# Kernel tuning notes

Hardware: AMD Instinct MI355X
Metric: run time of the kernel (lower is better)

## Reference

```python
import jax, jax.numpy as jnp
import numpy as np

NUM_HEADS = 16
EMBED_DIM = 1024
HEAD_DIM = EMBED_DIM // NUM_HEADS
SCALE = HEAD_DIM * -0.5  # faithful to source: multiplicative, negative


def setup_inputs() -> dict:
    key = jax.random.key(0)
    kx, kq, kk, kv, ko = jax.random.split(key, 5)
    B, S, E = 2, 2048, EMBED_DIM
    std = 1.0 / np.sqrt(E)
    return {
        "x": jax.random.normal(kx, (B, S, E), dtype=jnp.float32),
        "Wq": jax.random.normal(kq, (E, E), dtype=jnp.float32) * std,
        "Wk": jax.random.normal(kk, (E, E), dtype=jnp.float32) * std,
        "Wv": jax.random.normal(kv, (E, E), dtype=jnp.float32) * std,
        "Wo": jax.random.normal(ko, (E, E), dtype=jnp.float32) * std,
    }


def reference(x, Wq, Wk, Wv, Wo):
    B, S, E = x.shape
    H, D = NUM_HEADS, HEAD_DIM
    # nn.Linear(bias=False): y = x @ W.T
    q = (x @ Wq.T).reshape(B, S, H, D).transpose(0, 2, 1, 3)  # unused downstream (faithful to source)
    k = (x @ Wk.T).reshape(B, S, H, D).transpose(0, 2, 1, 3)  # [B,H,S,D]
    v = (x @ Wv.T).reshape(B, S, H, D).transpose(0, 2, 1, 3)
    # Source bug reproduced: logits = K @ V^T, scaled by head_dim * -0.5
    logits = jnp.einsum('bhsd,bhtd->bhst', k, v) * SCALE  # [B,H,S,S]
    attn = jax.nn.softmax(logits, axis=-1)
    out = jnp.einsum('bhst,bhtd->bhsd', attn, v)  # [B,H,S,D]
    out = out.transpose(0, 2, 1, 3).reshape(B, S, E)
    return out @ Wo.T
```

## Files before the change

### kernel.cpp

```cpp
#include <hip/hip_runtime.h>
#include <math.h>

#define B_ 2
#define S_ 2048
#define E_ 1024
#define H_ 16
#define D_ 64
#define M_ (B_ * S_)
#define SC2 (-46.166241308446828f)

typedef unsigned short u16;
typedef _Float16 f16;
typedef __attribute__((ext_vector_type(8))) _Float16 f16x8;
typedef __attribute__((ext_vector_type(2))) __fp16 fp16x2_n;
typedef __attribute__((ext_vector_type(16))) float f32x16;

static __device__ __forceinline__ f32x16 mfma_h(f16x8 a, f16x8 b, f32x16 c) {
    return __builtin_amdgcn_mfma_f32_32x32x16_f16(a, b, c, 0, 0, 0);
}
static __device__ __forceinline__ u16 f16bits(f16 h) {
    union { f16 h; u16 u; } c; c.h = h; return c.u;
}
static __device__ __forceinline__ unsigned pack2(u16 a, u16 b) {
    return (unsigned)a | ((unsigned)b << 16);
}
static __device__ __forceinline__ unsigned pkrtz(float a, float b) {
    fp16x2_n h = __builtin_amdgcn_cvt_pkrtz(a, b);
    unsigned u; __builtin_memcpy(&u, &h, 4); return u;
}
#define ROWMAP(r, hh) (((r) & 3) + ((((r) >> 2)) << 3) + ((hh) << 2))

__global__ __launch_bounds__(256)
void convert_split(const float* __restrict__ x, const float* __restrict__ Wk,
                   const float* __restrict__ Wv, const float* __restrict__ Wo,
                   u16* __restrict__ Xh, u16* __restrict__ Xl,
                   u16* __restrict__ Wkh, u16* __restrict__ Wkl,
                   u16* __restrict__ Wvh, u16* __restrict__ Wvl,
                   u16* __restrict__ Woh, u16* __restrict__ Wol)
{
    const int blk = blockIdx.x;
    const float* src; u16 *dh, *dl; int base; float sc = 1.0f;
    if (blk < 4096)      { src = x;  dh = Xh;  dl = Xl;  base = blk; }
    else if (blk < 5120) { src = Wk; dh = Wkh; dl = Wkl; base = blk - 4096; sc = SC2; }
    else if (blk < 6144) { src = Wv; dh = Wvh; dl = Wvl; base = blk - 5120; }
    else                 { src = Wo; dh = Woh; dl = Wol; base = blk - 6144; }
    const size_t off = ((size_t)base * 256 + threadIdx.x) * 4;
    const float4 v = *(const float4*)(src + off);
    const float f[4] = {v.x * sc, v.y * sc, v.z * sc, v.w * sc};
    u16 h4[4], l4[4];
#pragma unroll
    for (int i = 0; i < 4; ++i) {
        const f16 h = (f16)f[i];
        h4[i] = f16bits(h);
        l4[i] = f16bits((f16)(f[i] - (float)h));
    }
    *(uint2*)(dh + off) = make_uint2(pack2(h4[0], h4[1]), pack2(h4[2], h4[3]));
    *(uint2*)(dl + off) = make_uint2(pack2(l4[0], l4[1]), pack2(l4[2], l4[3]));
}

#define CSB 1032
#define ARR (4 * CSB)

template<int MODE>
__global__ __launch_bounds__(256, 1)
void gemm_f(const u16* __restrict__ Ah_, const u16* __restrict__ Al_,
            const u16* __restrict__ B1h_, const u16* __restrict__ B1l_,
            const u16* __restrict__ B2h_, const u16* __restrict__ B2l_,
            u16* __restrict__ Khg, u16* __restrict__ Klg,
            u16* __restrict__ Vhg, u16* __restrict__ Vtg,
            float* __restrict__ Cout)
{
    constexpr int NARR = (MODE == 0 ? 6 : 2);
    __shared__ u16 stage[NARR * ARR];

    const int tid = threadIdx.x;
    const int w = tid >> 6, l31 = tid & 31, hh = (tid >> 5) & 1;
    const int ws = w >> 1;
    const int wn = (w & 1) << 6;
    const int m0 = blockIdx.y * 128, n0 = blockIdx.x * 128;
    const int ch8 = (ws << 1) + hh;

    const int sr = tid >> 1, c0 = (tid & 1) << 1;
    const size_t gA = (size_t)(m0 + sr) * E_ + (c0 << 3);
    const size_t gB = (size_t)(n0 + sr) * E_ + (c0 << 3);
    const int lo0 = c0 * CSB + sr * 8;
    const int lo1 = (c0 + 1) * CSB + sr * 8;

    f32x16 acc1[4][2], acc2[4][2];
#pragma unroll
    for (int mt = 0; mt < 4; ++mt)
#pragma unroll
        for (int nt = 0; nt < 2; ++nt)
#pragma unroll
            for (int r = 0; r < 16; ++r) {
                acc1[mt][nt][r] = 0.f;
                if constexpr (MODE == 0) acc2[mt][nt][r] = 0.f;
            }

    f16x8 pf[2 * NARR];
    const u16* gptr[6];
    gptr[0] = Ah_; gptr[1] = Al_; gptr[2] = B1h_;
    gptr[3] = B1l_; gptr[4] = B2h_; gptr[5] = B2l_;

    auto load_tile = [&](int k0) {
#pragma unroll
        for (int a = 0; a < NARR; ++a) {
            const size_t g = ((MODE == 0 && a < 2) || (MODE == 1 && a < 1)) ? gA : gB;
            const u16* p = (MODE == 1 && a == 1) ? B1h_ : gptr[a];
            pf[2 * a + 0] = *(const f16x8*)(p + g + k0);
            pf[2 * a + 1] = *(const f16x8*)(p + g + k0 + 8);
        }
    };
    auto store_tile = [&]() {
#pragma unroll
        for (int a = 0; a < NARR; ++a) {
            *(f16x8*)&stage[a * ARR + lo0] = pf[2 * a + 0];
            *(f16x8*)&stage[a * ARR + lo1] = pf[2 * a + 1];
        }
    };

    load_tile(0);
    for (int it = 0; it < 32; ++it) {
        store_tile();
        __syncthreads();
        if (it + 1 < 32) load_tile((it + 1) << 5);

        f16x8 xh[4], xl[4];
#pragma unroll
        for (int mt = 0; mt < 4; ++mt) {
            const int off = ch8 * CSB + ((mt << 5) + l31) * 8;
            xh[mt] = *(const f16x8*)&stage[0 * ARR + off];
            if constexpr (MODE == 0)
                xl[mt] = *(const f16x8*)&stage[1 * ARR + off];
        }
#pragma unroll
        for (int nt = 0; nt < 2; ++nt) {
            const int boff = ch8 * CSB + (wn + (nt << 5) + l31) * 8;
            if constexpr (MODE == 0) {
                const f16x8 b1h = *(const f16x8*)&stage[2 * ARR + boff];
                const f16x8 b1l = *(const f16x8*)&stage[3 * ARR + boff];
                const f16x8 b2h = *(const f16x8*)&stage[4 * ARR + boff];
                const f16x8 b2l = *(const f16x8*)&stage[5 * ARR + boff];
#pragma unroll
                for (int mt = 0; mt < 4; ++mt) {
                    acc1[mt][nt] = mfma_h(xh[mt], b1h, acc1[mt][nt]);
                    acc1[mt][nt] = mfma_h(xh[mt], b1l, acc1[mt][nt]);
                    acc1[mt][nt] = mfma_h(xl[mt], b1h, acc1[mt][nt]);
                    acc2[mt][nt] = mfma_h(xh[mt], b2h, acc2[mt][nt]);
                    acc2[mt][nt] = mfma_h(xh[mt], b2l, acc2[mt][nt]);
                    acc2[mt][nt] = mfma_h(xl[mt], b2h, acc2[mt][nt]);
                }
            } else {
                const f16x8 b1h = *(const f16x8*)&stage[1 * ARR + boff];
#pragma unroll
                for (int mt = 0; mt < 4; ++mt)
                    acc1[mt][nt] = mfma_h(xh[mt], b1h, acc1[mt][nt]);
            }
        }
        __syncthreads();
    }

    float* red = (float*)stage;
#pragma unroll
    for (int ai = 0; ai < (MODE == 0 ? 2 : 1); ++ai) {
#pragma unroll
        for (int mt = 0; mt < 4; ++mt) {
            __syncthreads();
            if (ws == 1) {
#pragma unroll
                for (int nt = 0; nt < 2; ++nt)
#pragma unroll
                    for (int r = 0; r < 16; ++r)
                        red[ROWMAP(r, hh) * 128 + wn + (nt << 5) + l31] =
                            (ai == 0) ? acc1[mt][nt][r] : acc2[mt][nt][r];
            }
            __syncthreads();
            if (ws == 0) {
#pragma unroll
                for (int nt = 0; nt < 2; ++nt)
#pragma unroll
                    for (int r = 0; r < 16; ++r) {
                        const float p = red[ROWMAP(r, hh) * 128 + wn + (nt << 5) + l31];
                        if (ai == 0) acc1[mt][nt][r] += p; else acc2[mt][nt][r] += p;
                    }
            }
        }
    }
    if (ws != 0) return;

#pragma unroll
    for (int nt = 0; nt < 2; ++nt) {
        const int n = n0 + wn + (nt << 5) + l31;
        if constexpr (MODE == 1) {
#pragma unroll
            for (int mt = 0; mt < 4; ++mt)
#pragma unroll
                for (int r = 0; r < 16; ++r) {
                    const int m = m0 + (mt << 5) + ROWMAP(r, hh);
                    Cout[(size_t)m * E_ + n] = acc1[mt][nt][r];
                }
        } else {
            const int hd = n >> 6, d = n & 63;
            const int b = m0 >> 11;
#pragma unroll
            for (int mt = 0; mt < 4; ++mt) {
                u16 vb[16];
#pragma unroll
                for (int r = 0; r < 16; ++r) {
                    const int s = (m0 + (mt << 5) + ROWMAP(r, hh)) & (S_ - 1);
                    const size_t ib = (((size_t)(b * H_ + hd) << 11) + s) * D_ + d;
                    const float kv = acc1[mt][nt][r];
                    const f16 kh = (f16)kv;
                    Khg[ib] = f16bits(kh);
                    Klg[ib] = f16bits((f16)(kv - (float)kh));
                    const f16 vh = (f16)acc2[mt][nt][r];
                    vb[r] = f16bits(vh);
                    Vhg[ib] = vb[r];
                }
                const size_t vtb = ((size_t)(b * H_ + hd) * D_ + d) << 11;
#pragma unroll
                for (int g = 0; g < 4; ++g) {
                    const int s0 = ((m0 + (mt << 5)) & (S_ - 1)) + (g << 3) + (hh << 2);
                    *(uint2*)&Vtg[vtb + s0] =
                        make_uint2(pack2(vb[4 * g], vb[4 * g + 1]),
                                   pack2(vb[4 * g + 2], vb[4 * g + 3]));
                }
            }
        }
    }
}

#define CSA 520
#define VA  (8 * CSA)
#define CSP 264
#define PW  (8 * CSP)

__global__ __launch_bounds__(512, 2)
void attn_mfma(const u16* __restrict__ Kh, const u16* __restrict__ Kl,
               const u16* __restrict__ Vh, const u16* __restrict__ Vt,
               u16* __restrict__ Obuf)
{
    __shared__ u16 sV[2 * VA];
    __shared__ u16 sP[8][PW];
    __shared__ float Alpha[8][32], Linv[8][32];

    const int tid = threadIdx.x;
    const int w = tid >> 6, l31 = tid & 31, hh = (tid >> 5) & 1;
    const int bh = blockIdx.y;
    const int sbase = blockIdx.x * 256 + (w << 5);
    const int sg = sbase + l31;

    f16x8 kfh[4], kfl[4];
    {
        const size_t kb = ((size_t)bh * S_ + sg) * D_;
#pragma unroll
        for (int ks = 0; ks < 4; ++ks) {
            const int db = (ks << 4) + (hh << 3);
            kfh[ks] = *(const f16x8*)(Kh + kb + db);
            kfl[ks] = *(const f16x8*)(Kl + kb + db);
        }
    }

    f32x16 oacc[2];
#pragma unroll
    for (int r = 0; r < 16; ++r) { oacc[0][r] = 0.f; oacc[1][r] = 0.f; }
    float m_i = -INFINITY, l_i = 0.f;

    const int rr = tid >> 3, cc = tid & 7;
    const size_t gn = ((size_t)bh * S_ + rr) * D_ + (cc << 3);
    const size_t gt = ((size_t)bh * D_ + rr) * S_ + (cc << 3);
    const int slo = cc * CSA + rr * 8;
    u16* P = &sP[w][0];

    f16x8 pv[2];
    auto load_tile = [&](int t0) {
        pv[0] = *(const f16x8*)(Vh + gn + (size_t)t0 * D_);
        pv[1] = *(const f16x8*)(Vt + gt + t0);
    };

    load_tile(0);
    for (int it = 0; it < 32; ++it) {
        *(f16x8*)&sV[slo] = pv[0];
        *(f16x8*)&sV[VA + slo] = pv[1];
        __syncthreads();
        if (it + 1 < 32) load_tile((it + 1) << 6);

        f32x16 st[2];
#pragma unroll
        for (int r = 0; r < 16; ++r) { st[0][r] = 0.f; st[1][r] = 0.f; }
#pragma unroll
        for (int ks = 0; ks < 4; ++ks) {
            const int ch = (ks << 1) + hh;
#pragma unroll
            for (int mt = 0; mt < 2; ++mt) {
                const f16x8 av = *(const f16x8*)&sV[ch * CSA + ((mt << 5) + l31) * 8];
                st[mt] = mfma_h(av, kfh[ks], st[mt]);
                st[mt] = mfma_h(av, kfl[ks], st[mt]);
            }
        }

        float tmax = -INFINITY;
#pragma unroll
        for (int mt = 0; mt < 2; ++mt)
#pragma unroll
            for (int r = 0; r < 16; ++r) tmax = fmaxf(tmax, st[mt][r]);
        tmax = fmaxf(tmax, __shfl_xor(tmax, 32));
        const float mnew = fmaxf(m_i, tmax);
        const float alpha = __builtin_amdgcn_exp2f(m_i - mnew);
        m_i = mnew;
        const unsigned long long cmask = __ballot(tmax >= mnew - 30.f);

        if (cmask) {
            float rsum = 0.f;
#pragma unroll
            for (int mt = 0; mt < 2; ++mt)
#pragma unroll
                for (int r = 0; r < 16; ++r) {
                    const float p = __builtin_amdgcn_exp2f(st[mt][r] - mnew);
                    st[mt][r] = p;
                    rsum += p;
                }
            rsum += __shfl_xor(rsum, 32);
            l_i = l_i * alpha + rsum;
        }
        if (__ballot(alpha != 1.0f)) {
            if (hh == 0) Alpha[w][l31] = alpha;
#pragma unroll
            for (int g = 0; g < 4; ++g) {
                const float4 av = *(const float4*)&Alpha[w][(g << 3) + (hh << 2)];
                const float af[4] = {av.x, av.y, av.z, av.w};
#pragma unroll
                for (int q = 0; q < 4; ++q) {
                    oacc[0][(g << 2) + q] *= af[q];
                    oacc[1][(g << 2) + q] *= af[q];
                }
            }
        }
        if (cmask) {
#pragma unroll
            for (int mt = 0; mt < 2; ++mt)
#pragma unroll
                for (int g = 0; g < 4; ++g)
                    *(uint2*)&P[((mt << 2) + g) * CSP + l31 * 8 + (hh << 2)] =
                        make_uint2(pkrtz(st[mt][4 * g], st[mt][4 * g + 1]),
                                   pkrtz(st[mt][4 * g + 2], st[mt][4 * g + 3]));
#pragma unroll
            for (int ks = 0; ks < 4; ++ks) {
                const int ch = (ks << 1) + hh;
                const f16x8 pfr = *(const f16x8*)&P[ch * CSP + l31 * 8];
#pragma unroll
                for (int nt = 0; nt < 2; ++nt) {
                    const f16x8 vtf = *(const f16x8*)&sV[VA + ch * CSA + ((nt << 5) + l31) * 8];
                    oacc[nt] = mfma_h(pfr, vtf, oacc[nt]);
                }
            }
        }
        __syncthreads();
    }

    if (hh == 0) Linv[w][l31] = 1.0f / l_i;
    const int b = bh >> 4;
    const int hd = bh & 15;
    u16* Or = Obuf + ((size_t)b * S_ + sbase) * E_ + (hd << 6);
#pragma unroll
    for (int g = 0; g < 4; ++g) {
        const float4 iv = *(const float4*)&Linv[w][(g << 3) + (hh << 2)];
        const float invs[4] = {iv.x, iv.y, iv.z, iv.w};
#pragma unroll
        for (int nt = 0; nt < 2; ++nt)
#pragma unroll
            for (int q = 0; q < 4; ++q) {
                const int sl = (g << 3) + (hh << 2) + q;
                Or[(size_t)sl * E_ + (nt << 5) + l31] =
                    f16bits((f16)(oacc[nt][(g << 2) + q] * invs[q]));
            }
    }
}

extern "C" void kernel_launch(void* const* d_in, const int* in_sizes, int n_in,
                              void* d_out, int out_size, void* d_ws, size_t ws_size,
                              hipStream_t stream)
{
    (void)in_sizes; (void)n_in; (void)out_size; (void)ws_size;
    const float* x  = (const float*)d_in[0];
    const float* Wk = (const float*)d_in[2];
    const float* Wv = (const float*)d_in[3];
    const float* Wo = (const float*)d_in[4];
    float* out = (float*)d_out;

    char* ws = (char*)d_ws;
    const size_t MB = 1u << 20;
    u16* Xh  = (u16*)(ws + 0 * MB);
    u16* Xl  = (u16*)(ws + 8 * MB);
    u16* Wkh = (u16*)(ws + 16 * MB);
    u16* Wkl = (u16*)(ws + 18 * MB);
    u16* Wvh = (u16*)(ws + 20 * MB);
    u16* Wvl = (u16*)(ws + 22 * MB);
    u16* Woh = (u16*)(ws + 24 * MB);
    u16* Kh  = (u16*)(ws + 26 * MB);
    u16* Kl  = (u16*)(ws + 35 * MB);
    u16* Vh  = (u16*)(ws + 44 * MB);
    u16* Vt  = (u16*)(ws + 53 * MB);
    u16* Obuf = Xl;
    u16* Wol_junk = Kh;

    convert_split<<<7168, 256, 0, stream>>>(x, Wk, Wv, Wo,
                                            Xh, Xl, Wkh, Wkl, Wvh, Wvl, Woh, Wol_junk);
    gemm_f<0><<<dim3(E_ / 128, M_ / 128), 256, 0, stream>>>(
        Xh, Xl, Wkh, Wkl, Wvh, Wvl, Kh, Kl, Vh, Vt, nullptr);
    attn_mfma<<<dim3(S_ / 256, B_ * H_), 512, 0, stream>>>(Kh, Kl, Vh, Vt, Obuf);
    gemm_f<1><<<dim3(E_ / 128, M_ / 128), 256, 0, stream>>>(
        Obuf, Obuf, Woh, Woh, Woh, Woh,
        nullptr, nullptr, nullptr, nullptr, out);
}
```

Before: 239.2 us.

## Widen GEMM blocks to 512 threads, split K-score MFMA chains, skip Wo low-part writes

The projection GEMMs now launch 512 threads per block: four warps tile the 128x128 output 2x2 and two K-split groups each own half of every 32-wide K chunk, with a simplified cross-group reduction through shared memory. This gives each warp fewer accumulators and more warps per CU to hide latency, at the cost of an extra reduction pass. In attention, the hi and lo K MFMAs go into separate accumulators that are summed afterwards, which breaks the dependent MFMA chain. The convert kernel also stops writing the unused low half of Wo.

```diff
diff --git a/kernel.cpp b/kernel.cpp
--- a/kernel.cpp
+++ b/kernel.cpp
@@ -36,14 +36,14 @@
                    u16* __restrict__ Xh, u16* __restrict__ Xl,
                    u16* __restrict__ Wkh, u16* __restrict__ Wkl,
                    u16* __restrict__ Wvh, u16* __restrict__ Wvl,
-                   u16* __restrict__ Woh, u16* __restrict__ Wol)
+                   u16* __restrict__ Woh)
 {
     const int blk = blockIdx.x;
-    const float* src; u16 *dh, *dl; int base; float sc = 1.0f;
+    const float* src; u16 *dh, *dl; int base; float sc = 1.0f; bool wantlo = true;
     if (blk < 4096)      { src = x;  dh = Xh;  dl = Xl;  base = blk; }
     else if (blk < 5120) { src = Wk; dh = Wkh; dl = Wkl; base = blk - 4096; sc = SC2; }
     else if (blk < 6144) { src = Wv; dh = Wvh; dl = Wvl; base = blk - 5120; }
-    else                 { src = Wo; dh = Woh; dl = Wol; base = blk - 6144; }
+    else                 { src = Wo; dh = Woh; dl = Woh; base = blk - 6144; wantlo = false; }
     const size_t off = ((size_t)base * 256 + threadIdx.x) * 4;
     const float4 v = *(const float4*)(src + off);
     const float f[4] = {v.x * sc, v.y * sc, v.z * sc, v.w * sc};
@@ -55,40 +55,41 @@
         l4[i] = f16bits((f16)(f[i] - (float)h));
     }
     *(uint2*)(dh + off) = make_uint2(pack2(h4[0], h4[1]), pack2(h4[2], h4[3]));
-    *(uint2*)(dl + off) = make_uint2(pack2(l4[0], l4[1]), pack2(l4[2], l4[3]));
+    if (wantlo)
+        *(uint2*)(dl + off) = make_uint2(pack2(l4[0], l4[1]), pack2(l4[2], l4[3]));
 }
 
 #define CSB 1032
 #define ARR (4 * CSB)
 
 template<int MODE>
-__global__ __launch_bounds__(256, 1)
+__global__ __launch_bounds__(512, 2)
 void gemm_f(const u16* __restrict__ Ah_, const u16* __restrict__ Al_,
-            const u16* __restrict__ B1h_, const u16* __restrict__ B1l_,
-            const u16* __restrict__ B2h_, const u16* __restrict__ B2l_,
+            const u16* __restrict__ Bkh_, const u16* __restrict__ Bkl_,
+            const u16* __restrict__ Bvh_, const u16* __restrict__ Bvl_,
             u16* __restrict__ Khg, u16* __restrict__ Klg,
             u16* __restrict__ Vhg, u16* __restrict__ Vtg,
             float* __restrict__ Cout)
 {
     constexpr int NARR = (MODE == 0 ? 6 : 2);
-    __shared__ u16 stage[NARR * ARR];
+    constexpr int SSZ = (NARR * ARR > 16384 ? NARR * ARR : 16384);
+    __shared__ u16 stage[SSZ];
 
     const int tid = threadIdx.x;
     const int w = tid >> 6, l31 = tid & 31, hh = (tid >> 5) & 1;
-    const int ws = w >> 1;
-    const int wn = (w & 1) << 6;
+    const int wt = w & 3, ws = w >> 2;
+    const int wm = (wt >> 1) << 6, wn = (wt & 1) << 6;
     const int m0 = blockIdx.y * 128, n0 = blockIdx.x * 128;
     const int ch8 = (ws << 1) + hh;
 
-    const int sr = tid >> 1, c0 = (tid & 1) << 1;
-    const size_t gA = (size_t)(m0 + sr) * E_ + (c0 << 3);
-    const size_t gB = (size_t)(n0 + sr) * E_ + (c0 << 3);
-    const int lo0 = c0 * CSB + sr * 8;
-    const int lo1 = (c0 + 1) * CSB + sr * 8;
-
-    f32x16 acc1[4][2], acc2[4][2];
-#pragma unroll
-    for (int mt = 0; mt < 4; ++mt)
+    const int sr = tid >> 2, sch = tid & 3;
+    const size_t gA = (size_t)(m0 + sr) * E_ + (sch << 3);
+    const size_t gB = (size_t)(n0 + sr) * E_ + (sch << 3);
+    const int slo = sch * CSB + sr * 8;
+
+    f32x16 acc1[2][2], acc2[2][2];
+#pragma unroll
+    for (int mt = 0; mt < 2; ++mt)
 #pragma unroll
         for (int nt = 0; nt < 2; ++nt)
 #pragma unroll
@@ -97,26 +98,23 @@
                 if constexpr (MODE == 0) acc2[mt][nt][r] = 0.f;
             }
 
-    f16x8 pf[2 * NARR];
-    const u16* gptr[6];
-    gptr[0] = Ah_; gptr[1] = Al_; gptr[2] = B1h_;
-    gptr[3] = B1l_; gptr[4] = B2h_; gptr[5] = B2l_;
-
+    f16x8 pf[NARR];
     auto load_tile = [&](int k0) {
-#pragma unroll
-        for (int a = 0; a < NARR; ++a) {
-            const size_t g = ((MODE == 0 && a < 2) || (MODE == 1 && a < 1)) ? gA : gB;
-            const u16* p = (MODE == 1 && a == 1) ? B1h_ : gptr[a];
-            pf[2 * a + 0] = *(const f16x8*)(p + g + k0);
-            pf[2 * a + 1] = *(const f16x8*)(p + g + k0 + 8);
+        pf[0] = *(const f16x8*)(Ah_ + gA + k0);
+        if constexpr (MODE == 0) {
+            pf[1] = *(const f16x8*)(Al_ + gA + k0);
+            pf[2] = *(const f16x8*)(Bkh_ + gB + k0);
+            pf[3] = *(const f16x8*)(Bkl_ + gB + k0);
+            pf[4] = *(const f16x8*)(Bvh_ + gB + k0);
+            pf[5] = *(const f16x8*)(Bvl_ + gB + k0);
+        } else {
+            pf[1] = *(const f16x8*)(Bkh_ + gB + k0);
         }
     };
     auto store_tile = [&]() {
 #pragma unroll
-        for (int a = 0; a < NARR; ++a) {
-            *(f16x8*)&stage[a * ARR + lo0] = pf[2 * a + 0];
-            *(f16x8*)&stage[a * ARR + lo1] = pf[2 * a + 1];
-        }
+        for (int a = 0; a < NARR; ++a)
+            *(f16x8*)&stage[a * ARR + slo] = pf[a];
     };
 
     load_tile(0);
@@ -125,65 +123,63 @@
         __syncthreads();
         if (it + 1 < 32) load_tile((it + 1) << 5);
 
-        f16x8 xh[4], xl[4];
-#pragma unroll
-        for (int mt = 0; mt < 4; ++mt) {
-            const int off = ch8 * CSB + ((mt << 5) + l31) * 8;
+        const int co = ch8 * CSB;
+        f16x8 xh[2], xl[2];
+#pragma unroll
+        for (int mt = 0; mt < 2; ++mt) {
+            const int off = co + (wm + (mt << 5) + l31) * 8;
             xh[mt] = *(const f16x8*)&stage[0 * ARR + off];
             if constexpr (MODE == 0)
                 xl[mt] = *(const f16x8*)&stage[1 * ARR + off];
         }
 #pragma unroll
         for (int nt = 0; nt < 2; ++nt) {
-            const int boff = ch8 * CSB + (wn + (nt << 5) + l31) * 8;
+            const int ro = co + (wn + (nt << 5) + l31) * 8;
             if constexpr (MODE == 0) {
-                const f16x8 b1h = *(const f16x8*)&stage[2 * ARR + boff];
-                const f16x8 b1l = *(const f16x8*)&stage[3 * ARR + boff];
-                const f16x8 b2h = *(const f16x8*)&stage[4 * ARR + boff];
-                const f16x8 b2l = *(const f16x8*)&stage[5 * ARR + boff];
-#pragma unroll
-                for (int mt = 0; mt < 4; ++mt) {
-                    acc1[mt][nt] = mfma_h(xh[mt], b1h, acc1[mt][nt]);
-                    acc1[mt][nt] = mfma_h(xh[mt], b1l, acc1[mt][nt]);
-                    acc1[mt][nt] = mfma_h(xl[mt], b1h, acc1[mt][nt]);
-                    acc2[mt][nt] = mfma_h(xh[mt], b2h, acc2[mt][nt]);
-                    acc2[mt][nt] = mfma_h(xh[mt], b2l, acc2[mt][nt]);
-                    acc2[mt][nt] = mfma_h(xl[mt], b2h, acc2[mt][nt]);
+                const f16x8 bkh = *(const f16x8*)&stage[2 * ARR + ro];
+                const f16x8 bkl = *(const f16x8*)&stage[3 * ARR + ro];
+                const f16x8 bvh = *(const f16x8*)&stage[4 * ARR + ro];
+                const f16x8 bvl = *(const f16x8*)&stage[5 * ARR + ro];
+#pragma unroll
+                for (int mt = 0; mt < 2; ++mt) {
+                    acc1[mt][nt] = mfma_h(xh[mt], bkh, acc1[mt][nt]);
+                    acc1[mt][nt] = mfma_h(xh[mt], bkl, acc1[mt][nt]);
+                    acc1[mt][nt] = mfma_h(xl[mt], bkh, acc1[mt][nt]);
+                    acc2[mt][nt] = mfma_h(xh[mt], bvh, acc2[mt][nt]);
+                    acc2[mt][nt] = mfma_h(xh[mt], bvl, acc2[mt][nt]);
+                    acc2[mt][nt] = mfma_h(xl[mt], bvh, acc2[mt][nt]);
                 }
             } else {
-                const f16x8 b1h = *(const f16x8*)&stage[1 * ARR + boff];
-#pragma unroll
-                for (int mt = 0; mt < 4; ++mt)
-                    acc1[mt][nt] = mfma_h(xh[mt], b1h, acc1[mt][nt]);
+                const f16x8 bh = *(const f16x8*)&stage[1 * ARR + ro];
+#pragma unroll
+                for (int mt = 0; mt < 2; ++mt)
+                    acc1[mt][nt] = mfma_h(xh[mt], bh, acc1[mt][nt]);
             }
         }
         __syncthreads();
     }
 
     float* red = (float*)stage;
-#pragma unroll
-    for (int ai = 0; ai < (MODE == 0 ? 2 : 1); ++ai) {
-#pragma unroll
-        for (int mt = 0; mt < 4; ++mt) {
-            __syncthreads();
-            if (ws == 1) {
-#pragma unroll
-                for (int nt = 0; nt < 2; ++nt)
-#pragma unroll
-                    for (int r = 0; r < 16; ++r)
-                        red[ROWMAP(r, hh) * 128 + wn + (nt << 5) + l31] =
-                            (ai == 0) ? acc1[mt][nt][r] : acc2[mt][nt][r];
-            }
-            __syncthreads();
-            if (ws == 0) {
-#pragma unroll
-                for (int nt = 0; nt < 2; ++nt)
-#pragma unroll
-                    for (int r = 0; r < 16; ++r) {
-                        const float p = red[ROWMAP(r, hh) * 128 + wn + (nt << 5) + l31];
-                        if (ai == 0) acc1[mt][nt][r] += p; else acc2[mt][nt][r] += p;
-                    }
-            }
+    constexpr int NR = (MODE == 0 ? 4 : 2);
+#pragma unroll
+    for (int rd = 0; rd < NR; ++rd) {
+        const int mt = rd & 1;
+        f32x16 (*A)[2] = (MODE == 0 && rd >= 2) ? acc2 : acc1;
+        __syncthreads();
+        if (ws == 1) {
+#pragma unroll
+            for (int nt = 0; nt < 2; ++nt)
+#pragma unroll
+                for (int r = 0; r < 16; ++r)
+                    red[(((wt << 1) + nt) << 10) + (r << 6) + (hh << 5) + l31] = A[mt][nt][r];
+        }
+        __syncthreads();
+        if (ws == 0) {
+#pragma unroll
+            for (int nt = 0; nt < 2; ++nt)
+#pragma unroll
+                for (int r = 0; r < 16; ++r)
+                    A[mt][nt][r] += red[(((wt << 1) + nt) << 10) + (r << 6) + (hh << 5) + l31];
         }
     }
     if (ws != 0) return;
@@ -193,37 +189,37 @@
         const int n = n0 + wn + (nt << 5) + l31;
         if constexpr (MODE == 1) {
 #pragma unroll
-            for (int mt = 0; mt < 4; ++mt)
+            for (int mt = 0; mt < 2; ++mt)
 #pragma unroll
                 for (int r = 0; r < 16; ++r) {
-                    const int m = m0 + (mt << 5) + ROWMAP(r, hh);
+                    const int m = m0 + wm + (mt << 5) + ROWMAP(r, hh);
                     Cout[(size_t)m * E_ + n] = acc1[mt][nt][r];
                 }
         } else {
             const int hd = n >> 6, d = n & 63;
             const int b = m0 >> 11;
 #pragma unroll
-            for (int mt = 0; mt < 4; ++mt) {
-                u16 vb[16];
+            for (int mt = 0; mt < 2; ++mt) {
+                u16 vb16[16];
 #pragma unroll
                 for (int r = 0; r < 16; ++r) {
-                    const int s = (m0 + (mt << 5) + ROWMAP(r, hh)) & (S_ - 1);
+                    const int s = (m0 + wm + (mt << 5) + ROWMAP(r, hh)) & (S_ - 1);
                     const size_t ib = (((size_t)(b * H_ + hd) << 11) + s) * D_ + d;
                     const float kv = acc1[mt][nt][r];
                     const f16 kh = (f16)kv;
                     Khg[ib] = f16bits(kh);
                     Klg[ib] = f16bits((f16)(kv - (float)kh));
                     const f16 vh = (f16)acc2[mt][nt][r];
-                    vb[r] = f16bits(vh);
-                    Vhg[ib] = vb[r];
+                    vb16[r] = f16bits(vh);
+                    Vhg[ib] = vb16[r];
                 }
                 const size_t vtb = ((size_t)(b * H_ + hd) * D_ + d) << 11;
 #pragma unroll
                 for (int g = 0; g < 4; ++g) {
-                    const int s0 = ((m0 + (mt << 5)) & (S_ - 1)) + (g << 3) + (hh << 2);
+                    const int s0 = ((m0 + wm + (mt << 5)) & (S_ - 1)) + (g << 3) + (hh << 2);
                     *(uint2*)&Vtg[vtb + s0] =
-                        make_uint2(pack2(vb[4 * g], vb[4 * g + 1]),
-                                   pack2(vb[4 * g + 2], vb[4 * g + 3]));
+                        make_uint2(pack2(vb16[4 * g], vb16[4 * g + 1]),
+                                   pack2(vb16[4 * g + 2], vb16[4 * g + 3]));
                 }
             }
         }
@@ -285,25 +281,32 @@
         __syncthreads();
         if (it + 1 < 32) load_tile((it + 1) << 6);
 
-        f32x16 st[2];
-#pragma unroll
-        for (int r = 0; r < 16; ++r) { st[0][r] = 0.f; st[1][r] = 0.f; }
+        f32x16 sta[2], stb[2];
+#pragma unroll
+        for (int r = 0; r < 16; ++r) {
+            sta[0][r] = 0.f; sta[1][r] = 0.f;
+            stb[0][r] = 0.f; stb[1][r] = 0.f;
+        }
 #pragma unroll
         for (int ks = 0; ks < 4; ++ks) {
             const int ch = (ks << 1) + hh;
 #pragma unroll
             for (int mt = 0; mt < 2; ++mt) {
                 const f16x8 av = *(const f16x8*)&sV[ch * CSA + ((mt << 5) + l31) * 8];
-                st[mt] = mfma_h(av, kfh[ks], st[mt]);
-                st[mt] = mfma_h(av, kfl[ks], st[mt]);
-            }
-        }
+                sta[mt] = mfma_h(av, kfh[ks], sta[mt]);
+                stb[mt] = mfma_h(av, kfl[ks], stb[mt]);
+            }
+        }
+#pragma unroll
+        for (int mt = 0; mt < 2; ++mt)
+#pragma unroll
+            for (int r = 0; r < 16; ++r) sta[mt][r] += stb[mt][r];
 
         float tmax = -INFINITY;
 #pragma unroll
         for (int mt = 0; mt < 2; ++mt)
 #pragma unroll
-            for (int r = 0; r < 16; ++r) tmax = fmaxf(tmax, st[mt][r]);
+            for (int r = 0; r < 16; ++r) tmax = fmaxf(tmax, sta[mt][r]);
         tmax = fmaxf(tmax, __shfl_xor(tmax, 32));
         const float mnew = fmaxf(m_i, tmax);
         const float alpha = __builtin_amdgcn_exp2f(m_i - mnew);
@@ -316,8 +319,8 @@
             for (int mt = 0; mt < 2; ++mt)
 #pragma unroll
                 for (int r = 0; r < 16; ++r) {
-                    const float p = __builtin_amdgcn_exp2f(st[mt][r] - mnew);
-                    st[mt][r] = p;
+                    const float p = __builtin_amdgcn_exp2f(sta[mt][r] - mnew);
+                    sta[mt][r] = p;
                     rsum += p;
                 }
             rsum += __shfl_xor(rsum, 32);
@@ -342,8 +345,8 @@
 #pragma unroll
                 for (int g = 0; g < 4; ++g)
                     *(uint2*)&P[((mt << 2) + g) * CSP + l31 * 8 + (hh << 2)] =
-                        make_uint2(pkrtz(st[mt][4 * g], st[mt][4 * g + 1]),
-                                   pkrtz(st[mt][4 * g + 2], st[mt][4 * g + 3]));
+                        make_uint2(pkrtz(sta[mt][4 * g], sta[mt][4 * g + 1]),
+                                   pkrtz(sta[mt][4 * g + 2], sta[mt][4 * g + 3]));
 #pragma unroll
             for (int ks = 0; ks < 4; ++ks) {
                 const int ch = (ks << 1) + hh;
@@ -398,18 +401,17 @@
     u16* Wvl = (u16*)(ws + 22 * MB);
     u16* Woh = (u16*)(ws + 24 * MB);
     u16* Kh  = (u16*)(ws + 26 * MB);
-    u16* Kl  = (u16*)(ws + 35 * MB);
-    u16* Vh  = (u16*)(ws + 44 * MB);
-    u16* Vt  = (u16*)(ws + 53 * MB);
+    u16* Kl  = (u16*)(ws + 34 * MB);
+    u16* Vh  = (u16*)(ws + 42 * MB);
+    u16* Vt  = (u16*)(ws + 50 * MB);
     u16* Obuf = Xl;
-    u16* Wol_junk = Kh;
 
     convert_split<<<7168, 256, 0, stream>>>(x, Wk, Wv, Wo,
-                                            Xh, Xl, Wkh, Wkl, Wvh, Wvl, Woh, Wol_junk);
-    gemm_f<0><<<dim3(E_ / 128, M_ / 128), 256, 0, stream>>>(
+                                            Xh, Xl, Wkh, Wkl, Wvh, Wvl, Woh);
+    gemm_f<0><<<dim3(E_ / 128, M_ / 128), 512, 0, stream>>>(
         Xh, Xl, Wkh, Wkl, Wvh, Wvl, Kh, Kl, Vh, Vt, nullptr);
     attn_mfma<<<dim3(S_ / 256, B_ * H_), 512, 0, stream>>>(Kh, Kl, Vh, Vt, Obuf);
-    gemm_f<1><<<dim3(E_ / 128, M_ / 128), 256, 0, stream>>>(
+    gemm_f<1><<<dim3(E_ / 128, M_ / 128), 512, 0, stream>>>(
         Obuf, Obuf, Woh, Woh, Woh, Woh,
         nullptr, nullptr, nullptr, nullptr, out);
 }
```

After: 220.3 us. 1.09x faster.
